# Kernel optimization log

Measured on AMD Instinct MI355X. Metric: run time of the kernel, lower is better.

Reference implementation:

```python
import jax, jax.numpy as jnp
import numpy as np

B, S, K, N = 4, 2048, 4096, 4096


def setup_inputs() -> dict:
    key = jax.random.key(0)
    k1, k2, k3, k4 = jax.random.split(key, 4)
    x = jax.random.normal(k1, (B, S, K), dtype=jnp.float32)
    # int8 quantized weight values in [-128, 127], stored as int32 (jax-friendly container)
    qw = jax.random.randint(k2, (N, K), -128, 128, dtype=jnp.int32)
    # per-tensor scale: amax/127 style scalar
    sw = (jax.random.uniform(k3, (), dtype=jnp.float32) * 0.02 + 0.001)
    bias = jax.random.normal(k4, (N,), dtype=jnp.float32)
    return {"x": x, "qw": qw, "sw": sw, "bias": bias}


def reference(x, qw, sw, bias):
    # per_tensor_matmul: dequantize weight to fp32 with scalar scale, fp32 GEMM, cast back, add bias
    x_dtype = x.dtype
    w = qw.astype(jnp.float32) * sw          # [N, K] dequantized
    y = jnp.einsum('bsk,nk->bsn', x.astype(jnp.float32), w).astype(x_dtype)
    y = y + bias                              # [B, S, N]
    return y
```

## Files before the change

### kernel.cpp

```cpp
#include <hip/hip_runtime.h>
#include <stdint.h>

#define MDIM 8192
#define NDIM 4096
#define KDIM 4096

#define BM 128
#define BN 128
#define BK 64

typedef __attribute__((ext_vector_type(4)))  int i32x4;
typedef __attribute__((ext_vector_type(16))) int i32x16;

#define AS1 __attribute__((address_space(1)))
#define AS3 __attribute__((address_space(3)))

__device__ __forceinline__ int clamp127(int v) {
    return v > 127 ? 127 : (v < -127 ? -127 : v);
}

__global__ __launch_bounds__(256) void quant_x(
        const float* __restrict__ x, const float* __restrict__ sw,
        int8_t* __restrict__ Aq, float* __restrict__ scales) {
    const int row = blockIdx.x;
    const int t   = threadIdx.x;
    const float* xr = x + (size_t)row * KDIM;

    const float4* px = (const float4*)(xr + t * 16);
    float4 v0 = px[0], v1 = px[1], v2 = px[2], v3 = px[3];

    float a = fabsf(v0.x);
    a = fmaxf(a, fabsf(v0.y)); a = fmaxf(a, fabsf(v0.z)); a = fmaxf(a, fabsf(v0.w));
    a = fmaxf(a, fabsf(v1.x)); a = fmaxf(a, fabsf(v1.y)); a = fmaxf(a, fabsf(v1.z)); a = fmaxf(a, fabsf(v1.w));
    a = fmaxf(a, fabsf(v2.x)); a = fmaxf(a, fabsf(v2.y)); a = fmaxf(a, fabsf(v2.z)); a = fmaxf(a, fabsf(v2.w));
    a = fmaxf(a, fabsf(v3.x)); a = fmaxf(a, fabsf(v3.y)); a = fmaxf(a, fabsf(v3.z)); a = fmaxf(a, fabsf(v3.w));

    #pragma unroll
    for (int off = 32; off >= 1; off >>= 1)
        a = fmaxf(a, __shfl_xor(a, off));
    __shared__ float red[4];
    if ((t & 63) == 0) red[t >> 6] = a;
    __syncthreads();
    float amax = fmaxf(fmaxf(red[0], red[1]), fmaxf(red[2], red[3]));

    float inv = (amax > 0.f) ? (127.0f / amax) : 0.f;
    if (t == 0) scales[row] = (amax * (1.0f / 127.0f)) * (*sw);

    int b[16];
    b[ 0] = clamp127(__float2int_rn(v0.x * inv)); b[ 1] = clamp127(__float2int_rn(v0.y * inv));
    b[ 2] = clamp127(__float2int_rn(v0.z * inv)); b[ 3] = clamp127(__float2int_rn(v0.w * inv));
    b[ 4] = clamp127(__float2int_rn(v1.x * inv)); b[ 5] = clamp127(__float2int_rn(v1.y * inv));
    b[ 6] = clamp127(__float2int_rn(v1.z * inv)); b[ 7] = clamp127(__float2int_rn(v1.w * inv));
    b[ 8] = clamp127(__float2int_rn(v2.x * inv)); b[ 9] = clamp127(__float2int_rn(v2.y * inv));
    b[10] = clamp127(__float2int_rn(v2.z * inv)); b[11] = clamp127(__float2int_rn(v2.w * inv));
    b[12] = clamp127(__float2int_rn(v3.x * inv)); b[13] = clamp127(__float2int_rn(v3.y * inv));
    b[14] = clamp127(__float2int_rn(v3.z * inv)); b[15] = clamp127(__float2int_rn(v3.w * inv));

    i32x4 w;
    w[0] = (b[0]&255) | ((b[1]&255)<<8) | ((b[2]&255)<<16) | ((b[3]&255)<<24);
    w[1] = (b[4]&255) | ((b[5]&255)<<8) | ((b[6]&255)<<16) | ((b[7]&255)<<24);
    w[2] = (b[8]&255) | ((b[9]&255)<<8) | ((b[10]&255)<<16) | ((b[11]&255)<<24);
    w[3] = (b[12]&255)| ((b[13]&255)<<8)| ((b[14]&255)<<16)| ((b[15]&255)<<24);
    *(i32x4*)(Aq + (size_t)row * KDIM + t * 16) = w;
}

__global__ __launch_bounds__(256) void cvt_w(const int* __restrict__ qw, int8_t* __restrict__ Bq) {
    long i = (long)(blockIdx.x * blockDim.x + threadIdx.x) * 16;
    const int4* p = (const int4*)(qw + i);
    int4 a = p[0], b = p[1], c = p[2], d = p[3];
    i32x4 w;
    w[0] = (a.x&255) | ((a.y&255)<<8) | ((a.z&255)<<16) | ((a.w&255)<<24);
    w[1] = (b.x&255) | ((b.y&255)<<8) | ((b.z&255)<<16) | ((b.w&255)<<24);
    w[2] = (c.x&255) | ((c.y&255)<<8) | ((c.z&255)<<16) | ((c.w&255)<<24);
    w[3] = (d.x&255) | ((d.y&255)<<8) | ((d.z&255)<<16) | ((d.w&255)<<24);
    *(i32x4*)(Bq + i) = w;
}

__global__ __launch_bounds__(256) void gemm_bt_i8(
        const int8_t* __restrict__ A,
        const int8_t* __restrict__ Bm,
        const float* __restrict__ scales,
        const float* __restrict__ bias,
        float* __restrict__ C)
{
    __shared__ __align__(16) int8_t sA[BM * BK];
    __shared__ __align__(16) int8_t sB[BN * BK];

    const int tid  = threadIdx.x;
    const int wave = tid >> 6;
    const int lane = tid & 63;
    const int wr   = wave >> 1;
    const int wc   = wave & 1;
    const int l32  = lane & 31;
    const int hi   = lane >> 5;

    const int m0 = blockIdx.y * BM;
    const int n0 = blockIdx.x * BN;

    const int rS = wave * 16 + (lane >> 2);
    const int cS = ((lane & 3) ^ ((rS >> 1) & 3)) * 16;
    const int8_t* gA0 = A  + (size_t)(m0 + rS) * KDIM + cS;
    const int8_t* gA1 = gA0 + (size_t)64 * KDIM;
    const int8_t* gB0 = Bm + (size_t)(n0 + rS) * KDIM + cS;
    const int8_t* gB1 = gB0 + (size_t)64 * KDIM;
    int8_t* lA0 = sA + wave * 1024;
    int8_t* lA1 = lA0 + 4096;
    int8_t* lB0 = sB + wave * 1024;
    int8_t* lB1 = lB0 + 4096;

    const int swz = (l32 >> 1) & 3;
    const int co0 = ((hi    ) ^ swz) * 16;
    const int co1 = ((hi + 2) ^ swz) * 16;
    const int8_t* pA = sA + (wr * 64 + l32) * BK;
    const int8_t* pB = sB + (wc * 64 + l32) * BK;

    i32x16 acc[2][2];
#pragma unroll
    for (int i = 0; i < 2; i++)
#pragma unroll
        for (int j = 0; j < 2; j++)
#pragma unroll
            for (int r = 0; r < 16; r++) acc[i][j][r] = 0;

    for (int kt = 0; kt < KDIM; kt += BK) {
        __builtin_amdgcn_global_load_lds((AS1 const void*)(gA0 + kt), (AS3 void*)lA0, 16, 0, 0);
        __builtin_amdgcn_global_load_lds((AS1 const void*)(gA1 + kt), (AS3 void*)lA1, 16, 0, 0);
        __builtin_amdgcn_global_load_lds((AS1 const void*)(gB0 + kt), (AS3 void*)lB0, 16, 0, 0);
        __builtin_amdgcn_global_load_lds((AS1 const void*)(gB1 + kt), (AS3 void*)lB1, 16, 0, 0);
        __syncthreads();

        i32x4 a[2][2], b[2][2];
#pragma unroll
        for (int mi = 0; mi < 2; mi++) {
            a[mi][0] = *(const i32x4*)(pA + mi * 2048 + co0);
            a[mi][1] = *(const i32x4*)(pA + mi * 2048 + co1);
        }
#pragma unroll
        for (int ni = 0; ni < 2; ni++) {
            b[ni][0] = *(const i32x4*)(pB + ni * 2048 + co0);
            b[ni][1] = *(const i32x4*)(pB + ni * 2048 + co1);
        }

#pragma unroll
        for (int ks = 0; ks < 2; ks++)
#pragma unroll
            for (int mi = 0; mi < 2; mi++)
#pragma unroll
                for (int ni = 0; ni < 2; ni++)
                    acc[mi][ni] = __builtin_amdgcn_mfma_i32_32x32x32_i8(
                        a[mi][ks], b[ni][ks], acc[mi][ni], 0, 0, 0);

        __syncthreads();
    }

#pragma unroll
    for (int mi = 0; mi < 2; mi++) {
        const int row_base = m0 + wr * 64 + mi * 32 + 4 * hi;
        float sc[16];
#pragma unroll
        for (int r = 0; r < 16; r++)
            sc[r] = scales[row_base + (r & 3) + 8 * (r >> 2)];
#pragma unroll
        for (int ni = 0; ni < 2; ni++) {
            const int col = n0 + wc * 64 + ni * 32 + l32;
            const float bc = bias[col];
#pragma unroll
            for (int r = 0; r < 16; r++) {
                const int row = row_base + (r & 3) + 8 * (r >> 2);
                C[(size_t)row * NDIM + col] = (float)acc[mi][ni][r] * sc[r] + bc;
            }
        }
    }
}

__global__ void gemm_naive_f32(const float* __restrict__ x, const int* __restrict__ qw,
                               const float* __restrict__ sw, const float* __restrict__ bias,
                               float* __restrict__ out) {
    size_t id = (size_t)blockIdx.x * blockDim.x + threadIdx.x;
    if (id >= (size_t)MDIM * NDIM) return;
    int m = (int)(id / NDIM);
    int n = (int)(id % NDIM);
    const float* xr = x + (size_t)m * KDIM;
    const int*   wr = qw + (size_t)n * KDIM;
    float acc = 0.f;
    for (int k = 0; k < KDIM; k++) acc += xr[k] * (float)wr[k];
    out[id] = acc * (*sw) + bias[n];
}

extern "C" void kernel_launch(void* const* d_in, const int* in_sizes, int n_in,
                              void* d_out, int out_size, void* d_ws, size_t ws_size,
                              hipStream_t stream) {
    const float* x    = (const float*)d_in[0];
    const int*   qw   = (const int*)d_in[1];
    const float* sw   = (const float*)d_in[2];
    const float* bias = (const float*)d_in[3];
    float* out = (float*)d_out;

    const size_t needA = (size_t)MDIM * KDIM;
    const size_t needB = (size_t)NDIM * KDIM;
    const size_t needS = (size_t)MDIM * sizeof(float);

    if (ws_size >= needA + needB + needS) {
        int8_t* Aq = (int8_t*)d_ws;
        int8_t* Bq = Aq + needA;
        float*  scales = (float*)(Bq + needB);

        quant_x<<<MDIM, 256, 0, stream>>>(x, sw, Aq, scales);
        const long nw = (long)NDIM * KDIM;
        cvt_w<<<(int)(nw / (256 * 16)), 256, 0, stream>>>(qw, Bq);

        dim3 grid(NDIM / BN, MDIM / BM);
        gemm_bt_i8<<<grid, 256, 0, stream>>>(Aq, Bq, scales, bias, out);
    } else {
        size_t total = (size_t)MDIM * NDIM;
        gemm_naive_f32<<<(total + 255) / 256, 256, 0, stream>>>(x, qw, sw, bias, out);
    }
}
```

Before: 434.1 us.

## Double-buffer LDS in int8 GEMM and coalesce quantize/convert kernels

```diff
diff --git a/kernel.cpp b/kernel.cpp
--- a/kernel.cpp
+++ b/kernel.cpp
@@ -24,67 +24,54 @@
         int8_t* __restrict__ Aq, float* __restrict__ scales) {
     const int row = blockIdx.x;
     const int t   = threadIdx.x;
-    const float* xr = x + (size_t)row * KDIM;
-
-    const float4* px = (const float4*)(xr + t * 16);
-    float4 v0 = px[0], v1 = px[1], v2 = px[2], v3 = px[3];
-
-    float a = fabsf(v0.x);
-    a = fmaxf(a, fabsf(v0.y)); a = fmaxf(a, fabsf(v0.z)); a = fmaxf(a, fabsf(v0.w));
-    a = fmaxf(a, fabsf(v1.x)); a = fmaxf(a, fabsf(v1.y)); a = fmaxf(a, fabsf(v1.z)); a = fmaxf(a, fabsf(v1.w));
-    a = fmaxf(a, fabsf(v2.x)); a = fmaxf(a, fabsf(v2.y)); a = fmaxf(a, fabsf(v2.z)); a = fmaxf(a, fabsf(v2.w));
-    a = fmaxf(a, fabsf(v3.x)); a = fmaxf(a, fabsf(v3.y)); a = fmaxf(a, fabsf(v3.z)); a = fmaxf(a, fabsf(v3.w));
-
-    #pragma unroll
+    const float4* px = (const float4*)(x + (size_t)row * KDIM);
+
+    float4 v[4];
+#pragma unroll
+    for (int j = 0; j < 4; j++) v[j] = px[t + 256 * j];
+
+    float a = 0.f;
+#pragma unroll
+    for (int j = 0; j < 4; j++) {
+        a = fmaxf(a, fabsf(v[j].x)); a = fmaxf(a, fabsf(v[j].y));
+        a = fmaxf(a, fabsf(v[j].z)); a = fmaxf(a, fabsf(v[j].w));
+    }
+#pragma unroll
     for (int off = 32; off >= 1; off >>= 1)
         a = fmaxf(a, __shfl_xor(a, off));
     __shared__ float red[4];
     if ((t & 63) == 0) red[t >> 6] = a;
     __syncthreads();
-    float amax = fmaxf(fmaxf(red[0], red[1]), fmaxf(red[2], red[3]));
-
-    float inv = (amax > 0.f) ? (127.0f / amax) : 0.f;
+    const float amax = fmaxf(fmaxf(red[0], red[1]), fmaxf(red[2], red[3]));
+    const float inv  = (amax > 0.f) ? (127.0f / amax) : 0.f;
     if (t == 0) scales[row] = (amax * (1.0f / 127.0f)) * (*sw);
 
-    int b[16];
-    b[ 0] = clamp127(__float2int_rn(v0.x * inv)); b[ 1] = clamp127(__float2int_rn(v0.y * inv));
-    b[ 2] = clamp127(__float2int_rn(v0.z * inv)); b[ 3] = clamp127(__float2int_rn(v0.w * inv));
-    b[ 4] = clamp127(__float2int_rn(v1.x * inv)); b[ 5] = clamp127(__float2int_rn(v1.y * inv));
-    b[ 6] = clamp127(__float2int_rn(v1.z * inv)); b[ 7] = clamp127(__float2int_rn(v1.w * inv));
-    b[ 8] = clamp127(__float2int_rn(v2.x * inv)); b[ 9] = clamp127(__float2int_rn(v2.y * inv));
-    b[10] = clamp127(__float2int_rn(v2.z * inv)); b[11] = clamp127(__float2int_rn(v2.w * inv));
-    b[12] = clamp127(__float2int_rn(v3.x * inv)); b[13] = clamp127(__float2int_rn(v3.y * inv));
-    b[14] = clamp127(__float2int_rn(v3.z * inv)); b[15] = clamp127(__float2int_rn(v3.w * inv));
-
-    i32x4 w;
-    w[0] = (b[0]&255) | ((b[1]&255)<<8) | ((b[2]&255)<<16) | ((b[3]&255)<<24);
-    w[1] = (b[4]&255) | ((b[5]&255)<<8) | ((b[6]&255)<<16) | ((b[7]&255)<<24);
-    w[2] = (b[8]&255) | ((b[9]&255)<<8) | ((b[10]&255)<<16) | ((b[11]&255)<<24);
-    w[3] = (b[12]&255)| ((b[13]&255)<<8)| ((b[14]&255)<<16)| ((b[15]&255)<<24);
-    *(i32x4*)(Aq + (size_t)row * KDIM + t * 16) = w;
+    int* out32 = (int*)(Aq + (size_t)row * KDIM);
+#pragma unroll
+    for (int j = 0; j < 4; j++) {
+        int b0 = clamp127(__float2int_rn(v[j].x * inv));
+        int b1 = clamp127(__float2int_rn(v[j].y * inv));
+        int b2 = clamp127(__float2int_rn(v[j].z * inv));
+        int b3 = clamp127(__float2int_rn(v[j].w * inv));
+        out32[t + 256 * j] = (b0 & 255) | ((b1 & 255) << 8) | ((b2 & 255) << 16) | ((b3 & 255) << 24);
+    }
 }
 
 __global__ __launch_bounds__(256) void cvt_w(const int* __restrict__ qw, int8_t* __restrict__ Bq) {
-    long i = (long)(blockIdx.x * blockDim.x + threadIdx.x) * 16;
-    const int4* p = (const int4*)(qw + i);
-    int4 a = p[0], b = p[1], c = p[2], d = p[3];
-    i32x4 w;
-    w[0] = (a.x&255) | ((a.y&255)<<8) | ((a.z&255)<<16) | ((a.w&255)<<24);
-    w[1] = (b.x&255) | ((b.y&255)<<8) | ((b.z&255)<<16) | ((b.w&255)<<24);
-    w[2] = (c.x&255) | ((c.y&255)<<8) | ((c.z&255)<<16) | ((c.w&255)<<24);
-    w[3] = (d.x&255) | ((d.y&255)<<8) | ((d.z&255)<<16) | ((d.w&255)<<24);
-    *(i32x4*)(Bq + i) = w;
-}
-
-__global__ __launch_bounds__(256) void gemm_bt_i8(
+    const long i = (long)blockIdx.x * 256 + threadIdx.x;
+    int4 a = ((const int4*)qw)[i];
+    ((int*)Bq)[i] = (a.x & 255) | ((a.y & 255) << 8) | ((a.z & 255) << 16) | ((a.w & 255) << 24);
+}
+
+__global__ __launch_bounds__(256, 3) void gemm_bt_i8(
         const int8_t* __restrict__ A,
         const int8_t* __restrict__ Bm,
         const float* __restrict__ scales,
         const float* __restrict__ bias,
         float* __restrict__ C)
 {
-    __shared__ __align__(16) int8_t sA[BM * BK];
-    __shared__ __align__(16) int8_t sB[BN * BK];
+    __shared__ __align__(16) int8_t sA[2][BM * BK];
+    __shared__ __align__(16) int8_t sB[2][BN * BK];
 
     const int tid  = threadIdx.x;
     const int wave = tid >> 6;
@@ -103,16 +90,13 @@
     const int8_t* gA1 = gA0 + (size_t)64 * KDIM;
     const int8_t* gB0 = Bm + (size_t)(n0 + rS) * KDIM + cS;
     const int8_t* gB1 = gB0 + (size_t)64 * KDIM;
-    int8_t* lA0 = sA + wave * 1024;
-    int8_t* lA1 = lA0 + 4096;
-    int8_t* lB0 = sB + wave * 1024;
-    int8_t* lB1 = lB0 + 4096;
+    const int stoff = wave * 1024;
 
     const int swz = (l32 >> 1) & 3;
     const int co0 = ((hi    ) ^ swz) * 16;
     const int co1 = ((hi + 2) ^ swz) * 16;
-    const int8_t* pA = sA + (wr * 64 + l32) * BK;
-    const int8_t* pB = sB + (wc * 64 + l32) * BK;
+    const int rdA = (wr * 64 + l32) * BK;
+    const int rdB = (wc * 64 + l32) * BK;
 
     i32x16 acc[2][2];
 #pragma unroll
@@ -122,13 +106,15 @@
 #pragma unroll
             for (int r = 0; r < 16; r++) acc[i][j][r] = 0;
 
-    for (int kt = 0; kt < KDIM; kt += BK) {
-        __builtin_amdgcn_global_load_lds((AS1 const void*)(gA0 + kt), (AS3 void*)lA0, 16, 0, 0);
-        __builtin_amdgcn_global_load_lds((AS1 const void*)(gA1 + kt), (AS3 void*)lA1, 16, 0, 0);
-        __builtin_amdgcn_global_load_lds((AS1 const void*)(gB0 + kt), (AS3 void*)lB0, 16, 0, 0);
-        __builtin_amdgcn_global_load_lds((AS1 const void*)(gB1 + kt), (AS3 void*)lB1, 16, 0, 0);
-        __syncthreads();
-
+    auto prefetch = [&](int buf, int kt) {
+        __builtin_amdgcn_global_load_lds((AS1 const void*)(gA0 + kt), (AS3 void*)(&sA[buf][stoff]),        16, 0, 0);
+        __builtin_amdgcn_global_load_lds((AS1 const void*)(gA1 + kt), (AS3 void*)(&sA[buf][stoff + 4096]), 16, 0, 0);
+        __builtin_amdgcn_global_load_lds((AS1 const void*)(gB0 + kt), (AS3 void*)(&sB[buf][stoff]),        16, 0, 0);
+        __builtin_amdgcn_global_load_lds((AS1 const void*)(gB1 + kt), (AS3 void*)(&sB[buf][stoff + 4096]), 16, 0, 0);
+    };
+    auto compute = [&](int buf) {
+        const int8_t* pA = &sA[buf][rdA];
+        const int8_t* pB = &sB[buf][rdB];
         i32x4 a[2][2], b[2][2];
 #pragma unroll
         for (int mi = 0; mi < 2; mi++) {
@@ -140,7 +126,6 @@
             b[ni][0] = *(const i32x4*)(pB + ni * 2048 + co0);
             b[ni][1] = *(const i32x4*)(pB + ni * 2048 + co1);
         }
-
 #pragma unroll
         for (int ks = 0; ks < 2; ks++)
 #pragma unroll
@@ -149,9 +134,22 @@
                 for (int ni = 0; ni < 2; ni++)
                     acc[mi][ni] = __builtin_amdgcn_mfma_i32_32x32x32_i8(
                         a[mi][ks], b[ni][ks], acc[mi][ni], 0, 0, 0);
-
+    };
+
+    prefetch(0, 0);
+    for (int kt = 0; kt < KDIM - 2 * BK; kt += 2 * BK) {
         __syncthreads();
-    }
+        prefetch(1, kt + BK);
+        compute(0);
+        __syncthreads();
+        prefetch(0, kt + 2 * BK);
+        compute(1);
+    }
+    __syncthreads();
+    prefetch(1, KDIM - BK);
+    compute(0);
+    __syncthreads();
+    compute(1);
 
 #pragma unroll
     for (int mi = 0; mi < 2; mi++) {
@@ -206,8 +204,8 @@
         float*  scales = (float*)(Bq + needB);
 
         quant_x<<<MDIM, 256, 0, stream>>>(x, sw, Aq, scales);
-        const long nw = (long)NDIM * KDIM;
-        cvt_w<<<(int)(nw / (256 * 16)), 256, 0, stream>>>(qw, Bq);
+        const long nw4 = (long)NDIM * KDIM / 4;
+        cvt_w<<<(int)(nw4 / 256), 256, 0, stream>>>(qw, Bq);
 
         dim3 grid(NDIM / BN, MDIM / BM);
         gemm_bt_i8<<<grid, 256, 0, stream>>>(Aq, Bq, scales, bias, out);
```

Result: faster. 422.1 us (-2.8%).
